# Kernel tuning notes

Measured on AMD Instinct MI355X. Metric: run time of the kernel, lower is better.

Reference implementation:

```python
import jax, jax.numpy as jnp
import numpy as np
from jax.ops import segment_sum, segment_max

B, NPG, EPG = 2048, 32, 64          # graphs per drug, nodes/graph, edges/graph
N, E = B * NPG, B * EPG
FIN, EIN = 70, 6
HID, H, C = 128, 2, 64              # hidd_dim, conv heads, head_out_feats
NBLK, NCLASS = 4, 2
CAH, CAD = 8, 128                   # co-attention heads, dim_head


def _elu(x):
    return jnp.where(x > 0, x, jnp.expm1(x))


def _ln_graph(x, batch, w, b):
    # PyG LayerNorm(mode='graph'): normalize over all nodes+channels of each graph.
    cnt = jnp.float32(NPG * x.shape[1])  # all graphs have NPG nodes
    mean = segment_sum(x.sum(-1), batch, num_segments=B) / cnt
    xc = x - mean[batch][:, None]
    var = segment_sum((xc * xc).sum(-1), batch, num_segments=B) / cnt
    return xc * jax.lax.rsqrt(var + 1e-5)[batch][:, None] * w + b


def _ln(x, w, b):
    mu = x.mean(-1, keepdims=True)
    v = ((x - mu) ** 2).mean(-1, keepdims=True)
    return (x - mu) * jax.lax.rsqrt(v + 1e-5) * w + b


def _tconv(x, src, dst, ea, Wq, bq, Wk, bk, Wv, bv, We, Ws, bs):
    # PyG TransformerConv: edge-attention gather -> softmax over incoming edges -> scatter.
    q = (x @ Wq + bq).reshape(-1, H, C)
    k = (x @ Wk + bk).reshape(-1, H, C)
    v = (x @ Wv + bv).reshape(-1, H, C)
    e = (ea @ We).reshape(-1, H, C)
    kj = k[src] + e                                   # [E,H,C]
    a = (q[dst] * kj).sum(-1) * (C ** -0.5)           # [E,H]
    amax = segment_max(a, dst, num_segments=N)
    a = jnp.exp(a - amax[dst])
    a = a / (segment_sum(a, dst, num_segments=N)[dst] + 1e-16)
    out = segment_sum((v[src] + e) * a[:, :, None], dst, num_segments=N)
    return out.reshape(-1, H * C) + x @ Ws + bs       # root/skip connection


def _pool(x, src, dst, ea, batch, ebatch, w_rel, b_rel, w_root, W_re, b_re):
    # SAGPooling(min_score=-1): GraphConv score, per-graph softmax, all nodes kept,
    # then score-weighted global_add_pool; edge_attr pooled per graph and merged.
    agg = segment_sum(x[src], dst, num_segments=N)    # GraphConv 'add' aggregation
    score = agg @ w_rel + b_rel + x @ w_root          # [N]
    smax = segment_max(score, batch, num_segments=B)
    sexp = jnp.exp(score - smax[batch])
    score = sexp / (segment_sum(sexp, batch, num_segments=B)[batch] + 1e-16)
    g = segment_sum(x * score[:, None], batch, num_segments=B)      # [B,HID]
    ge = _elu(segment_sum(ea, ebatch, num_segments=B) @ W_re + b_re)
    g = g * ge
    return g / jnp.maximum(jnp.linalg.norm(g, axis=1, keepdims=True), 1e-12)


def _coattn(qx, kvx, lw, lb, Wq, Wkv, Wo):
    qx = _ln(qx, lw, lb)
    kvx = _ln(kvx, lw, lb)
    b, n = qx.shape[0], qx.shape[1]
    q = (qx @ Wq).reshape(b, n, CAH, CAD).transpose(0, 2, 1, 3)
    k, v = jnp.split(kvx @ Wkv, 2, axis=-1)
    k = k.reshape(b, n, CAH, CAD).transpose(0, 2, 1, 3)
    v = v.reshape(b, n, CAH, CAD).transpose(0, 2, 1, 3)
    attn = jax.nn.softmax(jnp.einsum('bhnd,bhmd->bhnm', q, k) * (CAD ** -0.5), axis=-1)
    o = jnp.einsum('bhnm,bhmd->bhnd', attn, v).transpose(0, 2, 1, 3).reshape(b, n, CAH * CAD)
    return o @ Wo


def setup_inputs() -> dict:
    key = jax.random.key(0)
    ks = iter(jax.random.split(key, 64))

    def nrm(shape, fan):
        return jax.random.normal(next(ks), shape, jnp.float32) * (fan ** -0.5)

    inp = {}
    inp['x1'] = jax.random.normal(next(ks), (N, FIN), jnp.float32)
    inp['x2'] = jax.random.normal(next(ks), (N, FIN), jnp.float32)
    inp['ea1'] = jax.random.normal(next(ks), (E, EIN), jnp.float32)
    inp['ea2'] = jax.random.normal(next(ks), (E, EIN), jnp.float32)
    inp['W_node'] = nrm((FIN, HID), FIN); inp['b_node'] = jnp.zeros((HID,), jnp.float32)
    inp['W_edge'] = nrm((EIN, 64), EIN); inp['b_edge'] = jnp.zeros((64,), jnp.float32)
    inp['ln0_w'] = jnp.ones((HID,), jnp.float32); inp['ln0_b'] = jnp.zeros((HID,), jnp.float32)
    inp['Wq'] = nrm((NBLK, 2, HID, HID), HID); inp['bq'] = jnp.zeros((NBLK, 2, HID), jnp.float32)
    inp['Wk'] = nrm((NBLK, 2, HID, HID), HID); inp['bk'] = jnp.zeros((NBLK, 2, HID), jnp.float32)
    inp['Wv'] = nrm((NBLK, 2, HID, HID), HID); inp['bv'] = jnp.zeros((NBLK, 2, HID), jnp.float32)
    inp['We'] = nrm((NBLK, 2, 64, HID), 64)
    inp['Ws'] = nrm((NBLK, 2, HID, HID), HID); inp['bs'] = jnp.zeros((NBLK, 2, HID), jnp.float32)
    inp['Wup'] = nrm((NBLK, 2, 64, 64), 64); inp['bup'] = jnp.zeros((NBLK, 2, 64), jnp.float32)
    inp['lnw'] = jnp.ones((NBLK, 2, HID), jnp.float32); inp['lnb'] = jnp.zeros((NBLK, 2, HID), jnp.float32)
    inp['w_rel'] = nrm((HID,), HID); inp['b_rel'] = jnp.zeros((), jnp.float32)
    inp['w_root'] = nrm((HID,), HID)
    inp['W_re'] = nrm((64, HID), 64); inp['b_re'] = jnp.zeros((HID,), jnp.float32)
    inp['ca_lw'] = jnp.ones((HID,), jnp.float32); inp['ca_lb'] = jnp.zeros((HID,), jnp.float32)
    inp['Wq_ca'] = nrm((HID, CAH * CAD), HID)
    inp['Wkv_ca'] = nrm((HID, 2 * CAH * CAD), HID)
    inp['Wo_ca'] = nrm((CAH * CAD, HID), CAH * CAD)
    inp['W_merge'] = nrm((NBLK * NBLK, NCLASS), NBLK * NBLK)
    inp['b_merge'] = jnp.zeros((NCLASS,), jnp.float32)
    off = jnp.repeat(jnp.arange(B, dtype=jnp.int32) * NPG, EPG)
    inp['edge_index1'] = jax.random.randint(next(ks), (2, E), 0, NPG, jnp.int32) + off[None, :]
    inp['edge_index2'] = jax.random.randint(next(ks), (2, E), 0, NPG, jnp.int32) + off[None, :]
    inp['batch1'] = jnp.repeat(jnp.arange(B, dtype=jnp.int32), NPG)
    inp['batch2'] = jnp.repeat(jnp.arange(B, dtype=jnp.int32), NPG)
    inp['ebatch1'] = jnp.repeat(jnp.arange(B, dtype=jnp.int32), EPG)
    inp['ebatch2'] = jnp.repeat(jnp.arange(B, dtype=jnp.int32), EPG)
    return inp


def reference(x1, x2, ea1, ea2, W_node, b_node, W_edge, b_edge, ln0_w, ln0_b,
              Wq, bq, Wk, bk, Wv, bv, We, Ws, bs, Wup, bup, lnw, lnb,
              w_rel, b_rel, w_root, W_re, b_re, ca_lw, ca_lb, Wq_ca, Wkv_ca, Wo_ca,
              W_merge, b_merge, edge_index1, edge_index2, batch1, batch2, ebatch1, ebatch2):
    s1, d1 = edge_index1[0], edge_index1[1]
    s2, d2 = edge_index2[0], edge_index2[1]
    x1 = _elu(_ln_graph(x1 @ W_node + b_node, batch1, ln0_w, ln0_b))
    x2 = _elu(_ln_graph(x2 @ W_node + b_node, batch2, ln0_w, ln0_b))
    ea1 = _elu(ea1 @ W_edge + b_edge)
    ea2 = _elu(ea2 @ W_edge + b_edge)

    def block(i, x, ea, src, dst, batch):
        x = _tconv(x, src, dst, ea, Wq[i, 0], bq[i, 0], Wk[i, 0], bk[i, 0],
                   Wv[i, 0], bv[i, 0], We[i, 0], Ws[i, 0], bs[i, 0])
        x = _elu(_ln_graph(x, batch, lnw[i, 0], lnb[i, 0]))
        ea = _elu(ea @ Wup[i, 0] + bup[i, 0])
        x = _tconv(x, src, dst, ea, Wq[i, 1], bq[i, 1], Wk[i, 1], bk[i, 1],
                   Wv[i, 1], bv[i, 1], We[i, 1], Ws[i, 1], bs[i, 1])
        ea_next = ea @ Wup[i, 1] + bup[i, 1]
        x = _elu(_ln_graph(x, batch, lnw[i, 1], lnb[i, 1]))
        return x, _elu(ea_next)

    hs, ts = [], []
    for i in range(NBLK):
        x1, ea1 = block(i, x1, ea1, s1, d1, batch1)
        x2, ea2 = block(i, x2, ea2, s2, d2, batch2)
        hs.append(_pool(x1, s1, d1, ea1, batch1, ebatch1, w_rel, b_rel, w_root, W_re, b_re))
        ts.append(_pool(x2, s2, d2, ea2, batch2, ebatch2, w_rel, b_rel, w_root, W_re, b_re))
    rh = jnp.stack(hs, 1)  # [B, NBLK, HID]
    rt = jnp.stack(ts, 1)
    ha = _coattn(rh, rt, ca_lw, ca_lb, Wq_ca, Wkv_ca, Wo_ca)
    ta = _coattn(rt, rh, ca_lw, ca_lb, Wq_ca, Wkv_ca, Wo_ca)
    m = jnp.einsum('bnd,bmd->bnm', ha, ta).reshape(ha.shape[0], NBLK * NBLK)
    return jax.nn.softmax(m @ W_merge + b_merge, axis=-1)
```

## Files before the change

### kernel.cpp

```cpp
#include <hip/hip_runtime.h>
#include <cstddef>
#include <cstdint>

#define NGRAPH 2048
#define NPG    32
#define EPG    64
#define NNODE  (NGRAPH*NPG)
#define NEDGE  (NGRAPH*EPG)
#define FINDIM 70
#define EINDIM 6
#define HID    128
#define NBLK   4
#define CAH    8
#define CAD    128
#define ES     68
#define XS     132

typedef __attribute__((ext_vector_type(8))) short bf16x8_t;
typedef __attribute__((ext_vector_type(4))) float f32x4;
typedef unsigned short ushortb;

#define MF3(accv, Ah_, Al_, Bh_, Bl_)                                          \
  accv = __builtin_amdgcn_mfma_f32_16x16x32_bf16(Ah_, Bh_, accv, 0, 0, 0);     \
  accv = __builtin_amdgcn_mfma_f32_16x16x32_bf16(Ah_, Bl_, accv, 0, 0, 0);     \
  accv = __builtin_amdgcn_mfma_f32_16x16x32_bf16(Al_, Bh_, accv, 0, 0, 0);

__device__ inline void split8(const float* p, bf16x8_t& h, bf16x8_t& l) {
  float4 v0 = *(const float4*)p, v1 = *(const float4*)(p + 4);
  float vv[8] = {v0.x, v0.y, v0.z, v0.w, v1.x, v1.y, v1.z, v1.w};
#pragma unroll
  for (int j = 0; j < 8; j++) {
    unsigned u = __builtin_bit_cast(unsigned, vv[j]);
    h[j] = (short)(u >> 16);
    float r = vv[j] - __builtin_bit_cast(float, u & 0xFFFF0000u);
    l[j] = (short)(__builtin_bit_cast(unsigned, r) >> 16);
  }
}

template<bool BIAS, bool ELU>
__global__ __launch_bounds__(256) void gemm_kernel(
    const float* __restrict__ A, const float* __restrict__ W,
    const float* __restrict__ bias, float* __restrict__ C,
    int M, int K, int Nc) {
  __shared__ float As[8][64];
  __shared__ float Bs[8][65];
  const int bm = blockIdx.y * 64, bn = blockIdx.x * 64;
  const int tid = threadIdx.x;
  const int tr = tid >> 4, tc = tid & 15;
  float acc[4][4];
#pragma unroll
  for (int i = 0; i < 4; i++)
#pragma unroll
    for (int j = 0; j < 4; j++) acc[i][j] = 0.f;
  for (int k0 = 0; k0 < K; k0 += 8) {
#pragma unroll
    for (int l = 0; l < 2; l++) {
      int idx = tid + l * 256;
      int r = idx >> 3, c = idx & 7;
      As[c][r] = (k0 + c < K) ? A[(size_t)(bm + r) * K + k0 + c] : 0.f;
      int rw = idx >> 6, cw = idx & 63;
      Bs[rw][cw] = (k0 + rw < K) ? W[(size_t)(k0 + rw) * Nc + bn + cw] : 0.f;
    }
    __syncthreads();
#pragma unroll
    for (int kk = 0; kk < 8; kk++) {
      float a_[4], w_[4];
#pragma unroll
      for (int i = 0; i < 4; i++) a_[i] = As[kk][tr * 4 + i];
#pragma unroll
      for (int j = 0; j < 4; j++) w_[j] = Bs[kk][tc * 4 + j];
#pragma unroll
      for (int i = 0; i < 4; i++)
#pragma unroll
        for (int j = 0; j < 4; j++) acc[i][j] += a_[i] * w_[j];
    }
    __syncthreads();
  }
#pragma unroll
  for (int i = 0; i < 4; i++) {
    int r = bm + tr * 4 + i;
#pragma unroll
    for (int j = 0; j < 4; j++) {
      int c = bn + tc * 4 + j;
      float v = acc[i][j];
      if (BIAS) v += bias[c];
      if (ELU) v = v > 0.f ? v : expm1f(v);
      C[(size_t)r * Nc + c] = v;
    }
  }
}

static void run_gemm(const float* A, const float* W, const float* bias, float* C,
                     int M, int K, int Nc, bool eluf, hipStream_t st) {
  dim3 grid(Nc / 64, M / 64), block(256);
  if (eluf) gemm_kernel<true, true><<<grid, block, 0, st>>>(A, W, bias, C, M, K, Nc);
  else      gemm_kernel<true, false><<<grid, block, 0, st>>>(A, W, bias, C, M, K, Nc);
}

__global__ void convw_kernel(const float* __restrict__ src, ushortb* __restrict__ h,
                             ushortb* __restrict__ l, int K, int N, int total,
                             int dstN, int nOff) {
  int idx = blockIdx.x * 256 + threadIdx.x;
  if (idx >= total) return;
  int k = idx % K;
  int t2 = idx / K;
  int n = t2 % N;
  int b = t2 / N;
  float v = src[((size_t)b * K + k) * N + n];
  unsigned uv = __builtin_bit_cast(unsigned, v);
  ushortb hb = (ushortb)(uv >> 16);
  float hf = __builtin_bit_cast(float, uv & 0xFFFF0000u);
  float rr = v - hf;
  ushortb lb = (ushortb)(__builtin_bit_cast(unsigned, rr) >> 16);
  size_t didx = ((size_t)b * dstN + nOff + n) * K + k;
  h[didx] = hb;
  l[didx] = lb;
}

__global__ void bcat_kernel(const float* __restrict__ bq, const float* __restrict__ bk,
                            const float* __restrict__ bv, float* __restrict__ o) {
  int t = blockIdx.x * 256 + threadIdx.x;
  if (t >= 8 * 384) return;
  int pi = t / 384, c = t % 384, sel = c >> 7, cc = c & 127;
  const float* s = sel == 0 ? bq : (sel == 1 ? bk : bv);
  o[t] = s[pi * 128 + cc];
}

__global__ __launch_bounds__(512) void gemm_mfma8_kernel(
    const float* __restrict__ A, const ushortb* __restrict__ Wh,
    const ushortb* __restrict__ Wl, float* __restrict__ C, int M, int K, int N) {
  __shared__ ushortb Ah[128 * 40];
  __shared__ ushortb Al[128 * 40];
  const int bm = blockIdx.y * 128, bn = blockIdx.x * 128;
  const int tid = threadIdx.x, lane = tid & 63, w = tid >> 6;
  const int wr = w >> 1, wc = w & 1;
  const int l16 = lane & 15, lk = lane >> 4;
  f32x4 acc[2][4];
#pragma unroll
  for (int m = 0; m < 2; m++)
#pragma unroll
    for (int n = 0; n < 4; n++) acc[m][n] = (f32x4)0.f;

  for (int k0 = 0; k0 < K; k0 += 32) {
    __syncthreads();
#pragma unroll
    for (int p = 0; p < 2; p++) {
      int base = p * 2048 + tid * 4;
      int r = base >> 5, c = base & 31;
      const float4 v = *(const float4*)(A + (size_t)(bm + r) * K + k0 + c);
      unsigned u0 = __builtin_bit_cast(unsigned, v.x);
      unsigned u1 = __builtin_bit_cast(unsigned, v.y);
      unsigned u2 = __builtin_bit_cast(unsigned, v.z);
      unsigned u3 = __builtin_bit_cast(unsigned, v.w);
      ushort4 hv;
      hv.x = (ushortb)(u0 >> 16); hv.y = (ushortb)(u1 >> 16);
      hv.z = (ushortb)(u2 >> 16); hv.w = (ushortb)(u3 >> 16);
      float r0 = v.x - __builtin_bit_cast(float, u0 & 0xFFFF0000u);
      float r1 = v.y - __builtin_bit_cast(float, u1 & 0xFFFF0000u);
      float r2 = v.z - __builtin_bit_cast(float, u2 & 0xFFFF0000u);
      float r3 = v.w - __builtin_bit_cast(float, u3 & 0xFFFF0000u);
      ushort4 lv;
      lv.x = (ushortb)(__builtin_bit_cast(unsigned, r0) >> 16);
      lv.y = (ushortb)(__builtin_bit_cast(unsigned, r1) >> 16);
      lv.z = (ushortb)(__builtin_bit_cast(unsigned, r2) >> 16);
      lv.w = (ushortb)(__builtin_bit_cast(unsigned, r3) >> 16);
      *(ushort4*)(&Ah[r * 40 + c]) = hv;
      *(ushort4*)(&Al[r * 40 + c]) = lv;
    }
    __syncthreads();
    bf16x8_t bh[4], bl[4];
#pragma unroll
    for (int n = 0; n < 4; n++) {
      size_t o = (size_t)(bn + wc * 64 + n * 16 + l16) * K + k0 + lk * 8;
      bh[n] = *(const bf16x8_t*)(Wh + o);
      bl[n] = *(const bf16x8_t*)(Wl + o);
    }
    bf16x8_t ah[2], al2[2];
#pragma unroll
    for (int m = 0; m < 2; m++) {
      int ao = (wr * 32 + m * 16 + l16) * 40 + lk * 8;
      ah[m]  = *(const bf16x8_t*)(&Ah[ao]);
      al2[m] = *(const bf16x8_t*)(&Al[ao]);
    }
#pragma unroll
    for (int m = 0; m < 2; m++)
#pragma unroll
      for (int n = 0; n < 4; n++) {
        MF3(acc[m][n], ah[m], al2[m], bh[n], bl[n]);
      }
  }
#pragma unroll
  for (int m = 0; m < 2; m++)
#pragma unroll
    for (int n = 0; n < 4; n++) {
      int col = bn + wc * 64 + n * 16 + l16;
#pragma unroll
      for (int r = 0; r < 4; r++) {
        int row = bm + wr * 32 + m * 16 + lk * 4 + r;
        C[(size_t)row * N + col] = acc[m][n][r];
      }
    }
}

static void run_mf8(const float* A, const ushortb* Wh, const ushortb* Wl,
                    float* C, int M, int K, int N, hipStream_t st) {
  dim3 grid(N / 128, M / 128), block(512);
  gemm_mfma8_kernel<<<grid, block, 0, st>>>(A, Wh, Wl, C, M, K, N);
}

__global__ void ln_graph_elu_kernel(const float* __restrict__ in, float* __restrict__ out,
                                    const float* __restrict__ w, const float* __restrict__ b) {
  const int g = blockIdx.x, t = threadIdx.x;
  const float* xg = in + (size_t)g * NPG * HID;
  float* og = out + (size_t)g * NPG * HID;
  float vals[16];
  float s = 0.f, ss = 0.f;
#pragma unroll
  for (int i = 0; i < 16; i++) {
    float v = xg[t + i * 256];
    vals[i] = v; s += v; ss += v * v;
  }
  __shared__ float ws0[4], ws1[4];
  for (int off = 32; off > 0; off >>= 1) { s += __shfl_down(s, off); ss += __shfl_down(ss, off); }
  int wid = t >> 6, lane = t & 63;
  if (lane == 0) { ws0[wid] = s; ws1[wid] = ss; }
  __syncthreads();
  if (t == 0) {
    float S = 0.f, SS = 0.f;
    for (int i = 0; i < 4; i++) { S += ws0[i]; SS += ws1[i]; }
    float mean = S / 4096.f;
    float var = SS / 4096.f - mean * mean;
    ws0[0] = mean; ws1[0] = rsqrtf(var + 1e-5f);
  }
  __syncthreads();
  float mean = ws0[0], inv = ws1[0];
#pragma unroll
  for (int i = 0; i < 16; i++) {
    int idx = t + i * 256;
    int ch = idx & 127;
    float y = (vals[i] - mean) * inv * w[ch] + b[ch];
    og[idx] = y > 0.f ? y : expm1f(y);
  }
}

template<bool POOL>
__global__ __launch_bounds__(256, 3) void mega_kernel(
    float* __restrict__ xb, float* __restrict__ ea,
    const ushortb* __restrict__ Wqkvh, const ushortb* __restrict__ Wqkvl,
    const ushortb* __restrict__ Wsh, const ushortb* __restrict__ Wsl,
    const ushortb* __restrict__ WeTh, const ushortb* __restrict__ WeTl,
    const ushortb* __restrict__ Wuph, const ushortb* __restrict__ Wupl,
    const float* __restrict__ bqkv_, const float* __restrict__ bs_,
    const float* __restrict__ bup_, const float* __restrict__ lnw_,
    const float* __restrict__ lnb_,
    const float* __restrict__ w_rel, const float* __restrict__ b_rel,
    const float* __restrict__ w_root, const float* __restrict__ W_re,
    const float* __restrict__ b_re, float* __restrict__ outp, int blk,
    const int* __restrict__ src, const int* __restrict__ dst) {
  const int g = blockIdx.x, t = threadIdx.x;
  const int lane = t & 63, w = t >> 6, l16 = lane & 15, lk = lane >> 4;
  __shared__ float el[EPG * ES];
  __shared__ float qs2[NPG * ES];
  __shared__ float ks2[NPG * ES];
  __shared__ unsigned char lists[NPG * EPG];
  __shared__ int deg_[NPG];
  __shared__ int sl[EPG], dl[EPG];
  __shared__ float alE[128];
  __shared__ float red0[NPG], red1[NPG];

  if (t < EPG) { sl[t] = src[g * EPG + t] - g * NPG; dl[t] = dst[g * EPG + t] - g * NPG; }
  if (t < NPG) {
    int c = 0;
    for (int e = 0; e < EPG; e++)
      if (dl[e] == t) lists[t * EPG + (c++)] = (unsigned char)e;
    deg_[t] = c;
  }

  bf16x8_t xh[2][4], xL[2][4];
#pragma unroll
  for (int m = 0; m < 2; m++)
#pragma unroll
    for (int kc = 0; kc < 4; kc++)
      split8(xb + ((size_t)g * NPG + m * 16 + l16) * HID + kc * 32 + lk * 8,
             xh[m][kc], xL[m][kc]);
  const float* eag = ea + ((size_t)g * EPG + w * 16 + l16) * 64;

  float accH0[8], accH1[8];
#pragma unroll
  for (int c = 0; c < 8; c++) { accH0[c] = 0.f; accH1[c] = 0.f; }

  auto proj = [&](int baseN, float* dstL) {
    f32x4 pa0 = (f32x4)0.f, pa1 = (f32x4)0.f;
#pragma unroll
    for (int kc = 0; kc < 4; kc++) {
      size_t o = (size_t)(baseN + w * 16 + l16) * HID + kc * 32 + lk * 8;
      bf16x8_t bh = *(const bf16x8_t*)(Wqkvh + o);
      bf16x8_t bl = *(const bf16x8_t*)(Wqkvl + o);
      MF3(pa0, xh[0][kc], xL[0][kc], bh, bl);
      MF3(pa1, xh[1][kc], xL[1][kc], bh, bl);
    }
    float bv = bqkv_[baseN + w * 16 + l16];
#pragma unroll
    for (int r = 0; r < 4; r++) {
      dstL[(lk * 4 + r) * ES + w * 16 + l16] = pa0[r] + bv;
      dstL[(16 + lk * 4 + r) * ES + w * 16 + l16] = pa1[r] + bv;
    }
  };

  auto head = [&](const int h, float (&acc8)[8]) {
    {
      bf16x8_t ea0h, ea0l, ea1h, ea1l;
      split8(eag + lk * 8, ea0h, ea0l);
      split8(eag + 32 + lk * 8, ea1h, ea1l);
#pragma unroll 1
      for (int n = 0; n < 4; n++) {
        f32x4 acc = (f32x4)0.f;
        size_t o0 = (size_t)(h * 64 + n * 16 + l16) * 64 + lk * 8;
        bf16x8_t bh0 = *(const bf16x8_t*)(WeTh + o0);
        bf16x8_t bl0 = *(const bf16x8_t*)(WeTl + o0);
        MF3(acc, ea0h, ea0l, bh0, bl0);
        bf16x8_t bh1 = *(const bf16x8_t*)(WeTh + o0 + 32);
        bf16x8_t bl1 = *(const bf16x8_t*)(WeTl + o0 + 32);
        MF3(acc, ea1h, ea1l, bh1, bl1);
#pragma unroll
        for (int r = 0; r < 4; r++)
          el[(w * 16 + lk * 4 + r) * ES + n * 16 + l16] = acc[r];
      }
    }
    proj(h * 64, qs2);
    proj(128 + h * 64, ks2);
    __syncthreads();
    {
      const int e2 = t >> 2, part = t & 3;
      const float* qp = qs2 + dl[e2] * ES + part * 16;
      const float* kp = ks2 + sl[e2] * ES + part * 16;
      const float* ep = el + e2 * ES + part * 16;
      float s = 0.f;
#pragma unroll
      for (int c = 0; c < 16; c += 4) {
        float4 qv = *(const float4*)(qp + c);
        float4 kv = *(const float4*)(kp + c);
        float4 ev = *(const float4*)(ep + c);
        s += qv.x * (kv.x + ev.x) + qv.y * (kv.y + ev.y) +
             qv.z * (kv.z + ev.z) + qv.w * (kv.w + ev.w);
      }
      s += __shfl_xor(s, 1);
      s += __shfl_xor(s, 2);
      if (part == 0) alE[e2] = s * 0.125f;
    }
    __syncthreads();
    f32x4 va0 = (f32x4)0.f, va1 = (f32x4)0.f;
#pragma unroll
    for (int kc = 0; kc < 4; kc++) {
      size_t o = (size_t)(256 + h * 64 + w * 16 + l16) * HID + kc * 32 + lk * 8;
      bf16x8_t bh = *(const bf16x8_t*)(Wqkvh + o);
      bf16x8_t bl = *(const bf16x8_t*)(Wqkvl + o);
      MF3(va0, xh[0][kc], xL[0][kc], bh, bl);
      MF3(va1, xh[1][kc], xL[1][kc], bh, bl);
    }
    {
      const int n = t >> 3, part = t & 7;
      float su = 0.f;
#pragma unroll 1
      for (int i = 0; i < 8; i++) {
        int e2 = part * 8 + i;
        if (dl[e2] == n) su += expf(alE[e2]);
      }
      su += __shfl_xor(su, 1);
      su += __shfl_xor(su, 2);
      su += __shfl_xor(su, 4);
      if (part == 0) red1[n] = su;
    }
    {
      float bv = bqkv_[256 + h * 64 + w * 16 + l16];
#pragma unroll
      for (int r = 0; r < 4; r++) {
        ks2[(lk * 4 + r) * ES + w * 16 + l16] = va0[r] + bv;
        ks2[(16 + lk * 4 + r) * ES + w * 16 + l16] = va1[r] + bv;
      }
    }
    __syncthreads();
    {
      const int n = t >> 3, cg = t & 7;
      const float inv = 1.f / (red1[n] + 1e-16f);
      const int dg = deg_[n];
      for (int i = 0; i < dg; i++) {
        const int e2 = lists[n * EPG + i];
        const float a = expf(alE[e2]) * inv;
        const float* vp = ks2 + sl[e2] * ES + cg * 8;
        const float* ep = el + e2 * ES + cg * 8;
        float4 v0 = *(const float4*)vp, v1 = *(const float4*)(vp + 4);
        float4 e0 = *(const float4*)ep, e1 = *(const float4*)(ep + 4);
        acc8[0] += a * (v0.x + e0.x); acc8[1] += a * (v0.y + e0.y);
        acc8[2] += a * (v0.z + e0.z); acc8[3] += a * (v0.w + e0.w);
        acc8[4] += a * (v1.x + e1.x); acc8[5] += a * (v1.y + e1.y);
        acc8[6] += a * (v1.z + e1.z); acc8[7] += a * (v1.w + e1.w);
      }
    }
    __syncthreads();
  };

  head(0, accH0);
  head(1, accH1);

  {
#pragma unroll
    for (int n = 0; n < 2; n++) {
      f32x4 sa0 = (f32x4)0.f, sa1 = (f32x4)0.f;
#pragma unroll
      for (int kc = 0; kc < 4; kc++) {
        size_t o = (size_t)(w * 32 + n * 16 + l16) * HID + kc * 32 + lk * 8;
        bf16x8_t bh = *(const bf16x8_t*)(Wsh + o);
        bf16x8_t bl = *(const bf16x8_t*)(Wsl + o);
        MF3(sa0, xh[0][kc], xL[0][kc], bh, bl);
        MF3(sa1, xh[1][kc], xL[1][kc], bh, bl);
      }
      int col = w * 32 + n * 16 + l16;
      float bv = bs_[col];
#pragma unroll
      for (int r = 0; r < 4; r++) {
        el[(lk * 4 + r) * XS + col] = sa0[r] + bv;
        el[(16 + lk * 4 + r) * XS + col] = sa1[r] + bv;
      }
    }
  }
  f32x4 ua[4];
  {
    bf16x8_t ea0h, ea0l, ea1h, ea1l;
    split8(eag + lk * 8, ea0h, ea0l);
    split8(eag + 32 + lk * 8, ea1h, ea1l);
#pragma unroll
    for (int n = 0; n < 4; n++) {
      f32x4 acc = (f32x4)0.f;
      size_t o0 = (size_t)(n * 16 + l16) * 64 + lk * 8;
      bf16x8_t bh0 = *(const bf16x8_t*)(Wuph + o0);
      bf16x8_t bl0 = *(const bf16x8_t*)(Wupl + o0);
      MF3(acc, ea0h, ea0l, bh0, bl0);
      bf16x8_t bh1 = *(const bf16x8_t*)(Wuph + o0 + 32);
      bf16x8_t bl1 = *(const bf16x8_t*)(Wupl + o0 + 32);
      MF3(acc, ea1h, ea1l, bh1, bl1);
      int col = n * 16 + l16;
      float bv = bup_[col];
#pragma unroll
      for (int r = 0; r < 4; r++) {
        float y = acc[r] + bv;
        y = y > 0.f ? y : expm1f(y);
        ua[n][r] = y;
        ea[((size_t)g * EPG + w * 16 + lk * 4 + r) * 64 + col] = y;
      }
    }
  }
  __syncthreads();
  {
    const int n = t >> 3, cg = t & 7;
    float v16[16];
#pragma unroll
    for (int c = 0; c < 8; c++) {
      v16[c] = accH0[c] + el[n * XS + cg * 8 + c];
      v16[8 + c] = accH1[c] + el[n * XS + 64 + cg * 8 + c];
    }
    float s = 0.f, ss = 0.f;
#pragma unroll
    for (int j = 0; j < 16; j++) { s += v16[j]; ss += v16[j] * v16[j]; }
    for (int o2 = 32; o2 > 0; o2 >>= 1) { s += __shfl_down(s, o2); ss += __shfl_down(ss, o2); }
    if (lane == 0) { red0[w] = s; red1[w] = ss; }
    __syncthreads();
    if (t == 0) {
      float S = red0[0] + red0[1] + red0[2] + red0[3];
      float SS = red1[0] + red1[1] + red1[2] + red1[3];
      float mean = S / 4096.f;
      float var = SS / 4096.f - mean * mean;
      red0[0] = mean; red1[0] = rsqrtf(var + 1e-5f);
    }
    __syncthreads();
    float mean = red0[0], inv = red1[0];
    float* xg = xb + (size_t)g * NPG * HID;
#pragma unroll
    for (int hh = 0; hh < 2; hh++)
#pragma unroll
      for (int c = 0; c < 8; c++) {
        int col = hh * 64 + cg * 8 + c;
        float y = (v16[hh * 8 + c] - mean) * inv * lnw_[col] + lnb_[col];
        y = y > 0.f ? y : expm1f(y);
        xg[n * HID + col] = y;
        el[n * XS + col] = y;
      }
  }

  if constexpr (POOL) {
    __syncthreads();
    {
#pragma unroll
      for (int n = 0; n < 4; n++) {
        float s = ua[n][0] + ua[n][1] + ua[n][2] + ua[n][3];
        s += __shfl_xor(s, 16);
        s += __shfl_xor(s, 32);
        if (lk == 0) qs2[w * 64 + n * 16 + l16] = s;
      }
      const int n = t >> 3, part = t & 7;
      float s = 0.f;
      for (int c = part * 16; c < part * 16 + 16; c++)
        s += el[n * XS + c] * w_root[c];
      const int dg = deg_[n];
      for (int i = 0; i < dg; i++) {
        int sn = sl[lists[n * EPG + i]];
        for (int c = part * 16; c < part * 16 + 16; c++)
          s += el[sn * XS + c] * w_rel[c];
      }
      s += __shfl_xor(s, 1);
      s += __shfl_xor(s, 2);
      s += __shfl_xor(s, 4);
      if (part == 0) alE[n] = s + b_rel[0];
    }
    __syncthreads();
    if (t < 64)
      alE[64 + t] = qs2[t] + qs2[64 + t] + qs2[128 + t] + qs2[192 + t];
    if (t >= 128 && t < 160) {
      int n = t - 128;
      float sc = alE[n];
      float m = sc;
      for (int o2 = 1; o2 <= 16; o2 <<= 1) m = fmaxf(m, __shfl_xor(m, o2));
      float e = expf(sc - m);
      float su = e;
      for (int o2 = 1; o2 <= 16; o2 <<= 1) su += __shfl_xor(su, o2);
      alE[n] = e / (su + 1e-16f);
    }
    __syncthreads();
    if (t < HID) {
      const int ch = t;
      float gv = 0.f;
      for (int n = 0; n < NPG; n++) gv += alE[n] * el[n * XS + ch];
      float s2 = b_re[ch];
      for (int k2 = 0; k2 < 64; k2++) s2 += alE[64 + k2] * W_re[k2 * HID + ch];
      s2 = s2 > 0.f ? s2 : expm1f(s2);
      float gl = gv * s2;
      el[4224 + ch] = gl;
      float sq = gl * gl;
      for (int o2 = 32; o2 > 0; o2 >>= 1) sq += __shfl_down(sq, o2);
      if (lane == 0) red0[w] = sq;
    }
    __syncthreads();
    if (t == 0) red1[0] = fmaxf(sqrtf(red0[0] + red0[1]), 1e-12f);
    __syncthreads();
    if (t < HID)
      outp[((size_t)g * NBLK + blk) * HID + t] = el[4224 + t] / red1[0];
  }
}

__global__ void ln_row_kernel(const float* __restrict__ in, float* __restrict__ out,
                              const float* __restrict__ w, const float* __restrict__ b) {
  const int r = blockIdx.x, t = threadIdx.x;
  float v = in[(size_t)r * HID + t];
  float s = v, ss = v * v;
  for (int off = 32; off > 0; off >>= 1) { s += __shfl_down(s, off); ss += __shfl_down(ss, off); }
  __shared__ float s0[2], s1[2];
  if ((t & 63) == 0) { s0[t >> 6] = s; s1[t >> 6] = ss; }
  __syncthreads();
  float S = s0[0] + s0[1], SS = s1[0] + s1[1];
  float mean = S / 128.f, var = SS / 128.f - mean * mean;
  out[(size_t)r * HID + t] = (v - mean) * rsqrtf(var + 1e-5f) * w[t] + b[t];
}

__global__ void coattn_kernel(const float* __restrict__ qb, const float* __restrict__ kvb,
                              float* __restrict__ ob) {
  const int bh = blockIdx.x, b = bh >> 3, h = bh & 7, t = threadIdx.x;
  __shared__ float attn[4][4];
  __shared__ float red[64];
  const int pair = t >> 2, part = t & 3;
  const int n = pair >> 2, m = pair & 3;
  const float* qp = qb + ((size_t)(b * 4 + n) * (CAH * CAD)) + h * CAD;
  const float* kp = kvb + ((size_t)(b * 4 + m) * (2 * CAH * CAD)) + h * CAD;
  float s = 0.f;
  for (int d = part * 32; d < part * 32 + 32; d++) s += qp[d] * kp[d];
  red[t] = s;
  __syncthreads();
  if (t < 16) {
    float sc = (red[t * 4] + red[t * 4 + 1] + red[t * 4 + 2] + red[t * 4 + 3]) * 0.08838834764831845f;
    attn[t >> 2][t & 3] = sc;
  }
  __syncthreads();
  if (t < 4) {
    float m_ = -1e30f;
    for (int j = 0; j < 4; j++) m_ = fmaxf(m_, attn[t][j]);
    float ex[4], su = 0.f;
    for (int j = 0; j < 4; j++) { ex[j] = expf(attn[t][j] - m_); su += ex[j]; }
    for (int j = 0; j < 4; j++) attn[t][j] = ex[j] / su;
  }
  __syncthreads();
  for (int i = t; i < 512; i += 64) {
    int n2 = i >> 7, d = i & 127;
    float acc = 0.f;
    for (int m2 = 0; m2 < 4; m2++)
      acc += attn[n2][m2] * kvb[((size_t)(b * 4 + m2) * (2 * CAH * CAD)) + CAH * CAD + h * CAD + d];
    ob[((size_t)(b * 4 + n2) * (CAH * CAD)) + h * CAD + d] = acc;
  }
}

__global__ void final_kernel(const float* __restrict__ ha, const float* __restrict__ ta,
                             const float* __restrict__ Wm, const float* __restrict__ bm,
                             float* __restrict__ out) {
  const int b = blockIdx.x, t = threadIdx.x;
  __shared__ float mm[16];
  if (t < 16) {
    int n = t >> 2, m2 = t & 3;
    const float* hp = ha + (size_t)(b * 4 + n) * HID;
    const float* tp = ta + (size_t)(b * 4 + m2) * HID;
    float s = 0.f;
    for (int c = 0; c < HID; c++) s += hp[c] * tp[c];
    mm[t] = s;
  }
  __syncthreads();
  if (t == 0) {
    float l0 = bm[0], l1 = bm[1];
    for (int j = 0; j < 16; j++) { l0 += mm[j] * Wm[j * 2]; l1 += mm[j] * Wm[j * 2 + 1]; }
    float m_ = fmaxf(l0, l1);
    float e0 = expf(l0 - m_), e1 = expf(l1 - m_);
    float su = e0 + e1;
    out[b * 2] = e0 / su;
    out[b * 2 + 1] = e1 / su;
  }
}

extern "C" void kernel_launch(void* const* d_in, const int* in_sizes, int n_in,
                              void* d_out, int out_size, void* d_ws, size_t ws_size,
                              hipStream_t stream) {
  const float* xin[2]  = {(const float*)d_in[0], (const float*)d_in[1]};
  const float* eain[2] = {(const float*)d_in[2], (const float*)d_in[3]};
  const float* W_node = (const float*)d_in[4];
  const float* b_node = (const float*)d_in[5];
  const float* W_edge = (const float*)d_in[6];
  const float* b_edge = (const float*)d_in[7];
  const float* ln0_w = (const float*)d_in[8];
  const float* ln0_b = (const float*)d_in[9];
  const float* Wq = (const float*)d_in[10];
  const float* bq = (const float*)d_in[11];
  const float* Wk = (const float*)d_in[12];
  const float* bk = (const float*)d_in[13];
  const float* Wv = (const float*)d_in[14];
  const float* bv = (const float*)d_in[15];
  const float* We = (const float*)d_in[16];
  const float* Wskip = (const float*)d_in[17];
  const float* bs = (const float*)d_in[18];
  const float* Wup = (const float*)d_in[19];
  const float* bup = (const float*)d_in[20];
  const float* lnw = (const float*)d_in[21];
  const float* lnb = (const float*)d_in[22];
  const float* w_rel = (const float*)d_in[23];
  const float* b_rel = (const float*)d_in[24];
  const float* w_root = (const float*)d_in[25];
  const float* W_re = (const float*)d_in[26];
  const float* b_re = (const float*)d_in[27];
  const float* ca_lw = (const float*)d_in[28];
  const float* ca_lb = (const float*)d_in[29];
  const float* Wq_ca = (const float*)d_in[30];
  const float* Wkv_ca = (const float*)d_in[31];
  const float* Wo_ca = (const float*)d_in[32];
  const float* W_merge = (const float*)d_in[33];
  const float* b_merge = (const float*)d_in[34];
  const int* ei[2] = {(const int*)d_in[35], (const int*)d_in[36]};
  float* out = (float*)d_out;
  (void)in_sizes; (void)n_in; (void)out_size;

  char* base = (char*)d_ws;
  size_t off = 0;
  auto alloc = [&](size_t elems) {
    float* r = (float*)(base + off);
    off += ((elems * 4 + 255) & ~(size_t)255);
    return r;
  };
  auto allocb = [&](size_t elems) {
    ushortb* r = (ushortb*)(base + off);
    off += ((elems * 2 + 255) & ~(size_t)255);
    return r;
  };
  float* xb  = alloc((size_t)NNODE * HID);
  float* ea  = alloc((size_t)NEDGE * 64);
  float* big = alloc((size_t)8192 * 2048);
  float* hs  = alloc((size_t)NGRAPH * NBLK * HID);
  float* ts  = alloc((size_t)NGRAPH * NBLK * HID);
  float* rhn = alloc((size_t)NGRAPH * NBLK * HID);
  float* rtn = alloc((size_t)NGRAPH * NBLK * HID);
  float* hab = alloc((size_t)NGRAPH * NBLK * HID);
  float* tab = alloc((size_t)NGRAPH * NBLK * HID);
  ushortb* Wqkvh = allocb((size_t)8 * 384 * 128); ushortb* Wqkvl = allocb((size_t)8 * 384 * 128);
  ushortb* Wsh = allocb(8 * 16384);  ushortb* Wsl = allocb(8 * 16384);
  ushortb* Wuph = allocb(8 * 4096);  ushortb* Wupl = allocb(8 * 4096);
  ushortb* WeTh = allocb(8 * 8192);  ushortb* WeTl = allocb(8 * 8192);
  ushortb* Wqcah = allocb(131072);   ushortb* Wqcal = allocb(131072);
  ushortb* Wkvh = allocb(262144);    ushortb* Wkvl = allocb(262144);
  ushortb* Woh = allocb(131072);     ushortb* Wol = allocb(131072);
  float* bqkv = alloc(8 * 384);
  if (off > ws_size) return;

  float* qc  = xb;
  float* kvc = big;
  float* oc  = ea;

  auto convw = [&](const float* s, ushortb* h, ushortb* l, int K, int N, int B,
                   int dstN, int nOff) {
    int tot = B * K * N;
    convw_kernel<<<(tot + 255) / 256, 256, 0, stream>>>(s, h, l, K, N, tot, dstN, nOff);
  };
  convw(Wq, Wqkvh, Wqkvl, 128, 128, 8, 384, 0);
  convw(Wk, Wqkvh, Wqkvl, 128, 128, 8, 384, 128);
  convw(Wv, Wqkvh, Wqkvl, 128, 128, 8, 384, 256);
  convw(Wskip, Wsh, Wsl, 128, 128, 8, 128, 0);
  convw(Wup, Wuph, Wupl, 64, 64, 8, 64, 0);
  convw(We, WeTh, WeTl, 64, 128, 8, 128, 0);
  convw(Wq_ca, Wqcah, Wqcal, 128, 1024, 1, 1024, 0);
  convw(Wkv_ca, Wkvh, Wkvl, 128, 2048, 1, 2048, 0);
  convw(Wo_ca, Woh, Wol, 1024, 128, 1, 128, 0);
  bcat_kernel<<<(8 * 384 + 255) / 256, 256, 0, stream>>>(bq, bk, bv, bqkv);

  for (int d2 = 0; d2 < 2; ++d2) {
    const int* src = ei[d2];
    const int* dst = ei[d2] + NEDGE;
    run_gemm(xin[d2], W_node, b_node, xb, NNODE, FINDIM, HID, false, stream);
    ln_graph_elu_kernel<<<NGRAPH, 256, 0, stream>>>(xb, xb, ln0_w, ln0_b);
    run_gemm(eain[d2], W_edge, b_edge, ea, NEDGE, EINDIM, 64, true, stream);
    float* outp = d2 == 0 ? hs : ts;
    for (int i = 0; i < NBLK; ++i) {
      int pi0 = i * 2, pi1 = i * 2 + 1;
      mega_kernel<false><<<NGRAPH, 256, 0, stream>>>(
          xb, ea,
          Wqkvh + (size_t)pi0 * 49152, Wqkvl + (size_t)pi0 * 49152,
          Wsh + (size_t)pi0 * 16384, Wsl + (size_t)pi0 * 16384,
          WeTh + (size_t)pi0 * 8192, WeTl + (size_t)pi0 * 8192,
          Wuph + (size_t)pi0 * 4096, Wupl + (size_t)pi0 * 4096,
          bqkv + pi0 * 384, bs + pi0 * 128, bup + pi0 * 64,
          lnw + pi0 * 128, lnb + pi0 * 128,
          w_rel, b_rel, w_root, W_re, b_re, nullptr, 0, src, dst);
      mega_kernel<true><<<NGRAPH, 256, 0, stream>>>(
          xb, ea,
          Wqkvh + (size_t)pi1 * 49152, Wqkvl + (size_t)pi1 * 49152,
          Wsh + (size_t)pi1 * 16384, Wsl + (size_t)pi1 * 16384,
          WeTh + (size_t)pi1 * 8192, WeTl + (size_t)pi1 * 8192,
          Wuph + (size_t)pi1 * 4096, Wupl + (size_t)pi1 * 4096,
          bqkv + pi1 * 384, bs + pi1 * 128, bup + pi1 * 64,
          lnw + pi1 * 128, lnb + pi1 * 128,
          w_rel, b_rel, w_root, W_re, b_re, outp, i, src, dst);
    }
  }

  ln_row_kernel<<<NGRAPH * NBLK, 128, 0, stream>>>(hs, rhn, ca_lw, ca_lb);
  ln_row_kernel<<<NGRAPH * NBLK, 128, 0, stream>>>(ts, rtn, ca_lw, ca_lb);
  run_mf8(rhn, Wqcah, Wqcal, qc, NGRAPH * NBLK, 128, 1024, stream);
  run_mf8(rtn, Wkvh, Wkvl, kvc, NGRAPH * NBLK, 128, 2048, stream);
  coattn_kernel<<<NGRAPH * CAH, 64, 0, stream>>>(qc, kvc, oc);
  run_mf8(oc, Woh, Wol, hab, NGRAPH * NBLK, 1024, 128, stream);
  run_mf8(rtn, Wqcah, Wqcal, qc, NGRAPH * NBLK, 128, 1024, stream);
  run_mf8(rhn, Wkvh, Wkvl, kvc, NGRAPH * NBLK, 128, 2048, stream);
  coattn_kernel<<<NGRAPH * CAH, 64, 0, stream>>>(qc, kvc, oc);
  run_mf8(oc, Woh, Wol, tab, NGRAPH * NBLK, 1024, 128, stream);

  final_kernel<<<NGRAPH, 64, 0, stream>>>(hab, tab, W_merge, b_merge, out);
}
```

Measured before the change: 3.420 ms.

## Process both attention heads concurrently with 512-thread blocks in mega kernel

Each graph's block grows from 256 to 512 threads. The two TransformerConv heads now run in parallel, one per half of the block, each with its own shared-memory slice, instead of being processed one after the other. The skip projection and the edge-update GEMM are also split across the two halves, and the per-head accumulators are merged through shared memory before the graph LayerNorm. This cuts the serialized per-graph work and the number of barriers, at the cost of more shared memory per block and tighter register limits under the new launch bounds.

Result: slower. 4.035 ms (+18.0%).

```diff
diff --git a/kernel.cpp b/kernel.cpp
--- a/kernel.cpp
+++ b/kernel.cpp
@@ -244,7 +244,7 @@
 }
 
 template<bool POOL>
-__global__ __launch_bounds__(256, 3) void mega_kernel(
+__global__ __launch_bounds__(512, 4) void mega_kernel(
     float* __restrict__ xb, float* __restrict__ ea,
     const ushortb* __restrict__ Wqkvh, const ushortb* __restrict__ Wqkvl,
     const ushortb* __restrict__ Wsh, const ushortb* __restrict__ Wsl,
@@ -259,14 +259,20 @@
     const int* __restrict__ src, const int* __restrict__ dst) {
   const int g = blockIdx.x, t = threadIdx.x;
   const int lane = t & 63, w = t >> 6, l16 = lane & 15, lk = lane >> 4;
-  __shared__ float el[EPG * ES];
-  __shared__ float qs2[NPG * ES];
-  __shared__ float ks2[NPG * ES];
+  const int h = w >> 2, wl = w & 3, tl = t & 255;
+  __shared__ float smem[4 * 4352];
   __shared__ unsigned char lists[NPG * EPG];
   __shared__ int deg_[NPG];
   __shared__ int sl[EPG], dl[EPG];
   __shared__ float alE[128];
-  __shared__ float red0[NPG], red1[NPG];
+  __shared__ float red1H[64];
+  __shared__ float redA[8], redB[8];
+  float* elh = smem + h * 4352;
+  float* qsh = smem + 8704 + h * 4352;
+  float* ksh = qsh + 2176;
+  float* accs = smem + 8704;
+  float* pa   = smem + 13056;
+  float* el0  = smem;
 
   if (t < EPG) { sl[t] = src[g * EPG + t] - g * NPG; dl[t] = dst[g * EPG + t] - g * NPG; }
   if (t < NPG) {
@@ -283,162 +289,172 @@
     for (int kc = 0; kc < 4; kc++)
       split8(xb + ((size_t)g * NPG + m * 16 + l16) * HID + kc * 32 + lk * 8,
              xh[m][kc], xL[m][kc]);
-  const float* eag = ea + ((size_t)g * EPG + w * 16 + l16) * 64;
-
-  float accH0[8], accH1[8];
-#pragma unroll
-  for (int c = 0; c < 8; c++) { accH0[c] = 0.f; accH1[c] = 0.f; }
-
-  auto proj = [&](int baseN, float* dstL) {
+  const float* eag = ea + ((size_t)g * EPG + wl * 16 + l16) * 64;
+  bf16x8_t efh[2], efl[2];
+  split8(eag + lk * 8, efh[0], efl[0]);
+  split8(eag + 32 + lk * 8, efh[1], efl[1]);
+
+  float acc8[8];
+#pragma unroll
+  for (int c = 0; c < 8; c++) acc8[c] = 0.f;
+
+  {
+#pragma unroll 1
+    for (int n = 0; n < 4; n++) {
+      f32x4 acc = (f32x4)0.f;
+      size_t o0 = (size_t)(h * 64 + n * 16 + l16) * 64 + lk * 8;
+      bf16x8_t bh0 = *(const bf16x8_t*)(WeTh + o0);
+      bf16x8_t bl0 = *(const bf16x8_t*)(WeTl + o0);
+      MF3(acc, efh[0], efl[0], bh0, bl0);
+      bf16x8_t bh1 = *(const bf16x8_t*)(WeTh + o0 + 32);
+      bf16x8_t bl1 = *(const bf16x8_t*)(WeTl + o0 + 32);
+      MF3(acc, efh[1], efl[1], bh1, bl1);
+#pragma unroll
+      for (int r = 0; r < 4; r++)
+        elh[(wl * 16 + lk * 4 + r) * ES + n * 16 + l16] = acc[r];
+    }
+  }
+  {
     f32x4 pa0 = (f32x4)0.f, pa1 = (f32x4)0.f;
 #pragma unroll
     for (int kc = 0; kc < 4; kc++) {
-      size_t o = (size_t)(baseN + w * 16 + l16) * HID + kc * 32 + lk * 8;
+      size_t o = (size_t)(h * 64 + wl * 16 + l16) * HID + kc * 32 + lk * 8;
       bf16x8_t bh = *(const bf16x8_t*)(Wqkvh + o);
       bf16x8_t bl = *(const bf16x8_t*)(Wqkvl + o);
       MF3(pa0, xh[0][kc], xL[0][kc], bh, bl);
       MF3(pa1, xh[1][kc], xL[1][kc], bh, bl);
     }
-    float bv = bqkv_[baseN + w * 16 + l16];
+    float bv = bqkv_[h * 64 + wl * 16 + l16];
 #pragma unroll
     for (int r = 0; r < 4; r++) {
-      dstL[(lk * 4 + r) * ES + w * 16 + l16] = pa0[r] + bv;
-      dstL[(16 + lk * 4 + r) * ES + w * 16 + l16] = pa1[r] + bv;
-    }
-  };
-
-  auto head = [&](const int h, float (&acc8)[8]) {
-    {
-      bf16x8_t ea0h, ea0l, ea1h, ea1l;
-      split8(eag + lk * 8, ea0h, ea0l);
-      split8(eag + 32 + lk * 8, ea1h, ea1l);
-#pragma unroll 1
-      for (int n = 0; n < 4; n++) {
-        f32x4 acc = (f32x4)0.f;
-        size_t o0 = (size_t)(h * 64 + n * 16 + l16) * 64 + lk * 8;
-        bf16x8_t bh0 = *(const bf16x8_t*)(WeTh + o0);
-        bf16x8_t bl0 = *(const bf16x8_t*)(WeTl + o0);
-        MF3(acc, ea0h, ea0l, bh0, bl0);
-        bf16x8_t bh1 = *(const bf16x8_t*)(WeTh + o0 + 32);
-        bf16x8_t bl1 = *(const bf16x8_t*)(WeTl + o0 + 32);
-        MF3(acc, ea1h, ea1l, bh1, bl1);
-#pragma unroll
-        for (int r = 0; r < 4; r++)
-          el[(w * 16 + lk * 4 + r) * ES + n * 16 + l16] = acc[r];
-      }
-    }
-    proj(h * 64, qs2);
-    proj(128 + h * 64, ks2);
-    __syncthreads();
-    {
-      const int e2 = t >> 2, part = t & 3;
-      const float* qp = qs2 + dl[e2] * ES + part * 16;
-      const float* kp = ks2 + sl[e2] * ES + part * 16;
-      const float* ep = el + e2 * ES + part * 16;
-      float s = 0.f;
-#pragma unroll
-      for (int c = 0; c < 16; c += 4) {
-        float4 qv = *(const float4*)(qp + c);
-        float4 kv = *(const float4*)(kp + c);
-        float4 ev = *(const float4*)(ep + c);
-        s += qv.x * (kv.x + ev.x) + qv.y * (kv.y + ev.y) +
-             qv.z * (kv.z + ev.z) + qv.w * (kv.w + ev.w);
-      }
-      s += __shfl_xor(s, 1);
-      s += __shfl_xor(s, 2);
-      if (part == 0) alE[e2] = s * 0.125f;
-    }
-    __syncthreads();
+      qsh[(lk * 4 + r) * ES + wl * 16 + l16] = pa0[r] + bv;
+      qsh[(16 + lk * 4 + r) * ES + wl * 16 + l16] = pa1[r] + bv;
+    }
+  }
+  {
+    f32x4 pa0 = (f32x4)0.f, pa1 = (f32x4)0.f;
+#pragma unroll
+    for (int kc = 0; kc < 4; kc++) {
+      size_t o = (size_t)(128 + h * 64 + wl * 16 + l16) * HID + kc * 32 + lk * 8;
+      bf16x8_t bh = *(const bf16x8_t*)(Wqkvh + o);
+      bf16x8_t bl = *(const bf16x8_t*)(Wqkvl + o);
+      MF3(pa0, xh[0][kc], xL[0][kc], bh, bl);
+      MF3(pa1, xh[1][kc], xL[1][kc], bh, bl);
+    }
+    float bv = bqkv_[128 + h * 64 + wl * 16 + l16];
+#pragma unroll
+    for (int r = 0; r < 4; r++) {
+      ksh[(lk * 4 + r) * ES + wl * 16 + l16] = pa0[r] + bv;
+      ksh[(16 + lk * 4 + r) * ES + wl * 16 + l16] = pa1[r] + bv;
+    }
+  }
+  __syncthreads();
+  {
+    const int e2 = tl >> 2, part = tl & 3;
+    const float* qp = qsh + dl[e2] * ES + part * 16;
+    const float* kp = ksh + sl[e2] * ES + part * 16;
+    const float* ep = elh + e2 * ES + part * 16;
+    float s = 0.f;
+#pragma unroll
+    for (int c = 0; c < 16; c += 4) {
+      float4 qv = *(const float4*)(qp + c);
+      float4 kv = *(const float4*)(kp + c);
+      float4 ev = *(const float4*)(ep + c);
+      s += qv.x * (kv.x + ev.x) + qv.y * (kv.y + ev.y) +
+           qv.z * (kv.z + ev.z) + qv.w * (kv.w + ev.w);
+    }
+    s += __shfl_xor(s, 1);
+    s += __shfl_xor(s, 2);
+    if (part == 0) alE[h * 64 + e2] = s * 0.125f;
+  }
+  __syncthreads();
+  {
     f32x4 va0 = (f32x4)0.f, va1 = (f32x4)0.f;
 #pragma unroll
     for (int kc = 0; kc < 4; kc++) {
-      size_t o = (size_t)(256 + h * 64 + w * 16 + l16) * HID + kc * 32 + lk * 8;
+      size_t o = (size_t)(256 + h * 64 + wl * 16 + l16) * HID + kc * 32 + lk * 8;
       bf16x8_t bh = *(const bf16x8_t*)(Wqkvh + o);
       bf16x8_t bl = *(const bf16x8_t*)(Wqkvl + o);
       MF3(va0, xh[0][kc], xL[0][kc], bh, bl);
       MF3(va1, xh[1][kc], xL[1][kc], bh, bl);
     }
     {
-      const int n = t >> 3, part = t & 7;
+      const int n = tl >> 3, part = tl & 7;
       float su = 0.f;
 #pragma unroll 1
       for (int i = 0; i < 8; i++) {
         int e2 = part * 8 + i;
-        if (dl[e2] == n) su += expf(alE[e2]);
+        if (dl[e2] == n) su += expf(alE[h * 64 + e2]);
       }
       su += __shfl_xor(su, 1);
       su += __shfl_xor(su, 2);
       su += __shfl_xor(su, 4);
-      if (part == 0) red1[n] = su;
-    }
-    {
-      float bv = bqkv_[256 + h * 64 + w * 16 + l16];
-#pragma unroll
-      for (int r = 0; r < 4; r++) {
-        ks2[(lk * 4 + r) * ES + w * 16 + l16] = va0[r] + bv;
-        ks2[(16 + lk * 4 + r) * ES + w * 16 + l16] = va1[r] + bv;
-      }
-    }
-    __syncthreads();
-    {
-      const int n = t >> 3, cg = t & 7;
-      const float inv = 1.f / (red1[n] + 1e-16f);
-      const int dg = deg_[n];
-      for (int i = 0; i < dg; i++) {
-        const int e2 = lists[n * EPG + i];
-        const float a = expf(alE[e2]) * inv;
-        const float* vp = ks2 + sl[e2] * ES + cg * 8;
-        const float* ep = el + e2 * ES + cg * 8;
-        float4 v0 = *(const float4*)vp, v1 = *(const float4*)(vp + 4);
-        float4 e0 = *(const float4*)ep, e1 = *(const float4*)(ep + 4);
-        acc8[0] += a * (v0.x + e0.x); acc8[1] += a * (v0.y + e0.y);
-        acc8[2] += a * (v0.z + e0.z); acc8[3] += a * (v0.w + e0.w);
-        acc8[4] += a * (v1.x + e1.x); acc8[5] += a * (v1.y + e1.y);
-        acc8[6] += a * (v1.z + e1.z); acc8[7] += a * (v1.w + e1.w);
-      }
-    }
-    __syncthreads();
-  };
-
-  head(0, accH0);
-  head(1, accH1);
-
+      if (part == 0) red1H[h * 32 + n] = su;
+    }
+    float bv = bqkv_[256 + h * 64 + wl * 16 + l16];
+#pragma unroll
+    for (int r = 0; r < 4; r++) {
+      ksh[(lk * 4 + r) * ES + wl * 16 + l16] = va0[r] + bv;
+      ksh[(16 + lk * 4 + r) * ES + wl * 16 + l16] = va1[r] + bv;
+    }
+  }
+  __syncthreads();
   {
+    const int n = tl >> 3, cg = tl & 7;
+    const float inv = 1.f / (red1H[h * 32 + n] + 1e-16f);
+    const int dg = deg_[n];
+    for (int i = 0; i < dg; i++) {
+      const int e2 = lists[n * EPG + i];
+      const float a = expf(alE[h * 64 + e2]) * inv;
+      const float* vp = ksh + sl[e2] * ES + cg * 8;
+      const float* ep = elh + e2 * ES + cg * 8;
+      float4 v0 = *(const float4*)vp, v1 = *(const float4*)(vp + 4);
+      float4 e0 = *(const float4*)ep, e1 = *(const float4*)(ep + 4);
+      acc8[0] += a * (v0.x + e0.x); acc8[1] += a * (v0.y + e0.y);
+      acc8[2] += a * (v0.z + e0.z); acc8[3] += a * (v0.w + e0.w);
+      acc8[4] += a * (v1.x + e1.x); acc8[5] += a * (v1.y + e1.y);
+      acc8[6] += a * (v1.z + e1.z); acc8[7] += a * (v1.w + e1.w);
+    }
+  }
+  __syncthreads();
+  {
+    const int n = tl >> 3, cg = tl & 7;
+#pragma unroll
+    for (int j = 0; j < 8; j++)
+      accs[n * XS + h * 64 + cg * 8 + j] = acc8[j];
+  }
+  f32x4 ua[4];
+  if (w >= 4) {
 #pragma unroll
     for (int n = 0; n < 2; n++) {
       f32x4 sa0 = (f32x4)0.f, sa1 = (f32x4)0.f;
 #pragma unroll
       for (int kc = 0; kc < 4; kc++) {
-        size_t o = (size_t)(w * 32 + n * 16 + l16) * HID + kc * 32 + lk * 8;
+        size_t o = (size_t)(wl * 32 + n * 16 + l16) * HID + kc * 32 + lk * 8;
         bf16x8_t bh = *(const bf16x8_t*)(Wsh + o);
         bf16x8_t bl = *(const bf16x8_t*)(Wsl + o);
         MF3(sa0, xh[0][kc], xL[0][kc], bh, bl);
         MF3(sa1, xh[1][kc], xL[1][kc], bh, bl);
       }
-      int col = w * 32 + n * 16 + l16;
+      int col = wl * 32 + n * 16 + l16;
       float bv = bs_[col];
 #pragma unroll
       for (int r = 0; r < 4; r++) {
-        el[(lk * 4 + r) * XS + col] = sa0[r] + bv;
-        el[(16 + lk * 4 + r) * XS + col] = sa1[r] + bv;
+        el0[(lk * 4 + r) * XS + col] = sa0[r] + bv;
+        el0[(16 + lk * 4 + r) * XS + col] = sa1[r] + bv;
       }
     }
-  }
-  f32x4 ua[4];
-  {
-    bf16x8_t ea0h, ea0l, ea1h, ea1l;
-    split8(eag + lk * 8, ea0h, ea0l);
-    split8(eag + 32 + lk * 8, ea1h, ea1l);
+  } else {
 #pragma unroll
     for (int n = 0; n < 4; n++) {
       f32x4 acc = (f32x4)0.f;
       size_t o0 = (size_t)(n * 16 + l16) * 64 + lk * 8;
       bf16x8_t bh0 = *(const bf16x8_t*)(Wuph + o0);
       bf16x8_t bl0 = *(const bf16x8_t*)(Wupl + o0);
-      MF3(acc, ea0h, ea0l, bh0, bl0);
+      MF3(acc, efh[0], efl[0], bh0, bl0);
       bf16x8_t bh1 = *(const bf16x8_t*)(Wuph + o0 + 32);
       bf16x8_t bl1 = *(const bf16x8_t*)(Wupl + o0 + 32);
-      MF3(acc, ea1h, ea1l, bh1, bl1);
+      MF3(acc, efh[1], efl[1], bh1, bl1);
       int col = n * 16 + l16;
       float bv = bup_[col];
 #pragma unroll
@@ -446,77 +462,76 @@
         float y = acc[r] + bv;
         y = y > 0.f ? y : expm1f(y);
         ua[n][r] = y;
-        ea[((size_t)g * EPG + w * 16 + lk * 4 + r) * 64 + col] = y;
+        ea[((size_t)g * EPG + wl * 16 + lk * 4 + r) * 64 + col] = y;
       }
     }
   }
   __syncthreads();
   {
-    const int n = t >> 3, cg = t & 7;
-    float v16[16];
-#pragma unroll
-    for (int c = 0; c < 8; c++) {
-      v16[c] = accH0[c] + el[n * XS + cg * 8 + c];
-      v16[8 + c] = accH1[c] + el[n * XS + 64 + cg * 8 + c];
-    }
+    const int n = t >> 4, sub = t & 15;
+    float v8[8];
     float s = 0.f, ss = 0.f;
 #pragma unroll
-    for (int j = 0; j < 16; j++) { s += v16[j]; ss += v16[j] * v16[j]; }
+    for (int j = 0; j < 8; j++) {
+      float v = accs[n * XS + sub * 8 + j] + el0[n * XS + sub * 8 + j];
+      v8[j] = v; s += v; ss += v * v;
+    }
     for (int o2 = 32; o2 > 0; o2 >>= 1) { s += __shfl_down(s, o2); ss += __shfl_down(ss, o2); }
-    if (lane == 0) { red0[w] = s; red1[w] = ss; }
+    if (lane == 0) { redA[w] = s; redB[w] = ss; }
     __syncthreads();
     if (t == 0) {
-      float S = red0[0] + red0[1] + red0[2] + red0[3];
-      float SS = red1[0] + red1[1] + red1[2] + red1[3];
+      float S = 0.f, SS = 0.f;
+      for (int i = 0; i < 8; i++) { S += redA[i]; SS += redB[i]; }
       float mean = S / 4096.f;
       float var = SS / 4096.f - mean * mean;
-      red0[0] = mean; red1[0] = rsqrtf(var + 1e-5f);
-    }
-    __syncthreads();
-    float mean = red0[0], inv = red1[0];
+      redA[0] = mean; redB[0] = rsqrtf(var + 1e-5f);
+    }
+    __syncthreads();
+    float mean = redA[0], inv = redB[0];
     float* xg = xb + (size_t)g * NPG * HID;
 #pragma unroll
-    for (int hh = 0; hh < 2; hh++)
-#pragma unroll
-      for (int c = 0; c < 8; c++) {
-        int col = hh * 64 + cg * 8 + c;
-        float y = (v16[hh * 8 + c] - mean) * inv * lnw_[col] + lnb_[col];
-        y = y > 0.f ? y : expm1f(y);
-        xg[n * HID + col] = y;
-        el[n * XS + col] = y;
-      }
+    for (int j = 0; j < 8; j++) {
+      int col = sub * 8 + j;
+      float y = (v8[j] - mean) * inv * lnw_[col] + lnb_[col];
+      y = y > 0.f ? y : expm1f(y);
+      xg[n * HID + col] = y;
+      el0[n * XS + col] = y;
+    }
   }
 
   if constexpr (POOL) {
     __syncthreads();
-    {
+    if (w < 4) {
 #pragma unroll
       for (int n = 0; n < 4; n++) {
         float s = ua[n][0] + ua[n][1] + ua[n][2] + ua[n][3];
         s += __shfl_xor(s, 16);
         s += __shfl_xor(s, 32);
-        if (lk == 0) qs2[w * 64 + n * 16 + l16] = s;
+        if (lk == 0) pa[w * 64 + n * 16 + l16] = s;
       }
-      const int n = t >> 3, part = t & 7;
+    }
+    {
+      const int n = t >> 4, part = t & 15;
       float s = 0.f;
-      for (int c = part * 16; c < part * 16 + 16; c++)
-        s += el[n * XS + c] * w_root[c];
+      for (int c = part * 8; c < part * 8 + 8; c++)
+        s += el0[n * XS + c] * w_root[c];
       const int dg = deg_[n];
       for (int i = 0; i < dg; i++) {
         int sn = sl[lists[n * EPG + i]];
-        for (int c = part * 16; c < part * 16 + 16; c++)
-          s += el[sn * XS + c] * w_rel[c];
+        for (int c = part * 8; c < part * 8 + 8; c++)
+          s += el0[sn * XS + c] * w_rel[c];
       }
       s += __shfl_xor(s, 1);
       s += __shfl_xor(s, 2);
       s += __shfl_xor(s, 4);
+      s += __shfl_xor(s, 8);
       if (part == 0) alE[n] = s + b_rel[0];
     }
     __syncthreads();
     if (t < 64)
-      alE[64 + t] = qs2[t] + qs2[64 + t] + qs2[128 + t] + qs2[192 + t];
-    if (t >= 128 && t < 160) {
-      int n = t - 128;
+      alE[64 + t] = pa[t] + pa[64 + t] + pa[128 + t] + pa[192 + t];
+    if (t >= 64 && t < 96) {
+      int n = t - 64;
       float sc = alE[n];
       float m = sc;
       for (int o2 = 1; o2 <= 16; o2 <<= 1) m = fmaxf(m, __shfl_xor(m, o2));
@@ -529,21 +544,21 @@
     if (t < HID) {
       const int ch = t;
       float gv = 0.f;
-      for (int n = 0; n < NPG; n++) gv += alE[n] * el[n * XS + ch];
+      for (int n = 0; n < NPG; n++) gv += alE[n] * el0[n * XS + ch];
       float s2 = b_re[ch];
       for (int k2 = 0; k2 < 64; k2++) s2 += alE[64 + k2] * W_re[k2 * HID + ch];
       s2 = s2 > 0.f ? s2 : expm1f(s2);
       float gl = gv * s2;
-      el[4224 + ch] = gl;
+      el0[4224 + ch] = gl;
       float sq = gl * gl;
       for (int o2 = 32; o2 > 0; o2 >>= 1) sq += __shfl_down(sq, o2);
-      if (lane == 0) red0[w] = sq;
-    }
-    __syncthreads();
-    if (t == 0) red1[0] = fmaxf(sqrtf(red0[0] + red0[1]), 1e-12f);
+      if (lane == 0) redA[w] = sq;
+    }
+    __syncthreads();
+    if (t == 0) redB[0] = fmaxf(sqrtf(redA[0] + redA[1]), 1e-12f);
     __syncthreads();
     if (t < HID)
-      outp[((size_t)g * NBLK + blk) * HID + t] = el[4224 + t] / red1[0];
+      outp[((size_t)g * NBLK + blk) * HID + t] = el0[4224 + t] / redB[0];
   }
 }
 
@@ -721,7 +736,7 @@
     float* outp = d2 == 0 ? hs : ts;
     for (int i = 0; i < NBLK; ++i) {
       int pi0 = i * 2, pi1 = i * 2 + 1;
-      mega_kernel<false><<<NGRAPH, 256, 0, stream>>>(
+      mega_kernel<false><<<NGRAPH, 512, 0, stream>>>(
           xb, ea,
           Wqkvh + (size_t)pi0 * 49152, Wqkvl + (size_t)pi0 * 49152,
           Wsh + (size_t)pi0 * 16384, Wsl + (size_t)pi0 * 16384,
@@ -730,7 +745,7 @@
           bqkv + pi0 * 384, bs + pi0 * 128, bup + pi0 * 64,
           lnw + pi0 * 128, lnb + pi0 * 128,
           w_rel, b_rel, w_root, W_re, b_re, nullptr, 0, src, dst);
-      mega_kernel<true><<<NGRAPH, 256, 0, stream>>>(
+      mega_kernel<true><<<NGRAPH, 512, 0, stream>>>(
           xb, ea,
           Wqkvh + (size_t)pi1 * 49152, Wqkvl + (size_t)pi1 * 49152,
           Wsh + (size_t)pi1 * 16384, Wsl + (size_t)pi1 * 16384,
```
